# Performance work log

Hardware: AMD Instinct MI355X
Metric: run time of the kernel (lower is better)

The kernel has to match this reference:

```python
import jax, jax.numpy as jnp
import numpy as np
import math

B, S, E, H = 2, 1024, 2560, 32
D = E // H  # 80


def setup_inputs() -> dict:
    key = jax.random.key(0)
    ks = jax.random.split(key, 10)
    hidden_states = jax.random.normal(ks[0], (B, S, E), dtype=jnp.float32)
    Wqkv = jax.random.normal(ks[1], (E, 3 * E), dtype=jnp.float32) * 0.02
    bqkv = jnp.zeros((3 * E,), dtype=jnp.float32)
    Wproj = jax.random.normal(ks[2], (E, E), dtype=jnp.float32) * 0.02
    bproj = jnp.zeros((E,), dtype=jnp.float32)
    # gate matrices: hadamard, pauli_x, pauli_z (all real branches in torch code)
    hadamard = jnp.array([[1.0, 1.0], [1.0, -1.0]], dtype=jnp.float32) / math.sqrt(2.0)
    pauli_x = jnp.array([[0.0, 1.0], [1.0, 0.0]], dtype=jnp.float32)
    pauli_z = jnp.array([[1.0, 0.0], [0.0, -1.0]], dtype=jnp.float32)
    gate_mats = jnp.stack([hadamard, pauli_x, pauli_z])  # (3,2,2)
    # phase_rotation init is zeros in torch; randomize slightly for nontrivial numerics
    gate_phases = jax.random.normal(ks[3], (3, D), dtype=jnp.float32) * 0.1
    gate_amps = jnp.ones((3, D), dtype=jnp.float32)
    quantum_phase = jax.random.normal(ks[4], (H,), dtype=jnp.float32) * 0.1
    interference_strength = jnp.float32(0.8)
    return {
        'hidden_states': hidden_states, 'Wqkv': Wqkv, 'bqkv': bqkv,
        'Wproj': Wproj, 'bproj': bproj, 'gate_mats': gate_mats,
        'gate_phases': gate_phases, 'gate_amps': gate_amps,
        'quantum_phase': quantum_phase,
        'interference_strength': interference_strength,
    }


def _gate_coeffs(gate_mats, gate_phases, gate_amps):
    # QuantumGate fwd: stack([x*cos(p), x*sin(p)], -1) @ G, summed over last axis, * amp
    # => per-dim scalar coeff: (cos(p)*(g00+g01) + sin(p)*(g10+g11)) * amp
    row0 = gate_mats[:, 0, 0] + gate_mats[:, 0, 1]  # (3,)
    row1 = gate_mats[:, 1, 0] + gate_mats[:, 1, 1]  # (3,)
    return (jnp.cos(gate_phases) * row0[:, None] + jnp.sin(gate_phases) * row1[:, None]) * gate_amps  # (3, D)


def reference(hidden_states, Wqkv, bqkv, Wproj, bproj, gate_mats, gate_phases, gate_amps, quantum_phase, interference_strength):
    scale = D ** -0.5
    qkv = hidden_states @ Wqkv + bqkv  # (B,S,3E)
    q, k, v = jnp.split(qkv, 3, axis=-1)
    # (B,H,S,D)
    q = q.reshape(B, S, H, D).transpose(0, 2, 1, 3)
    k = k.reshape(B, S, H, D).transpose(0, 2, 1, 3)
    v = v.reshape(B, S, H, D).transpose(0, 2, 1, 3)

    attn_scores = jnp.einsum('bhqd,bhkd->bhqk', q, k) * scale

    coeffs = _gate_coeffs(gate_mats, gate_phases, gate_amps)  # (3,D)
    # quantum attention per gate: (q * coeff_i) @ k^T * scale
    qa = jnp.einsum('gd,bhqd,bhkd->gbhqk', coeffs, q, k) * scale  # (3,B,H,S,S)
    interference = (qa[0] * qa[1] + qa[0] * qa[2] + qa[1] * qa[2]) * interference_strength
    attn_scores = attn_scores + interference / 3.0

    attn_probs = jax.nn.softmax(attn_scores, axis=-1)
    attn_probs = attn_probs * jnp.cos(quantum_phase)[None, :, None, None]

    attn_output = jnp.einsum('bhqk,bhkd->bhqd', attn_probs, v)
    attn_output = attn_output.transpose(0, 2, 1, 3).reshape(B, S, E)
    return attn_output @ Wproj + bproj
```

## Files before the change

kernel.cpp:

```cpp
#include <hip/hip_runtime.h>
#include <hip/hip_bf16.h>
#include <math.h>

#define S_  1024
#define E_  2560
#define H_  32
#define D_  80
#define E3_ 7680
#define M_  2048
#define QK_ 5120

typedef short bf16x8 __attribute__((ext_vector_type(8)));
typedef float f32x4  __attribute__((ext_vector_type(4)));

static __device__ __forceinline__ float bf2f(unsigned short u) {
    unsigned int i = ((unsigned int)u) << 16;
    float f; __builtin_memcpy(&f, &i, 4); return f;
}
static __device__ __forceinline__ unsigned short f2bf(float f) {
    unsigned int i; __builtin_memcpy(&i, &f, 4);
    i += 0x7fffu + ((i >> 16) & 1u);
    return (unsigned short)(i >> 16);
}

static __device__ __forceinline__ void gload_lds16(
    const unsigned short* g, unsigned short* l)
{
    __builtin_amdgcn_global_load_lds(
        (const __attribute__((address_space(1))) void*)g,
        (__attribute__((address_space(3))) void*)l, 16, 0, 0);
}

__global__ __launch_bounds__(256) void cvt_bf16_kernel(
    const float* __restrict__ in, unsigned short* __restrict__ out, int n8)
{
    int i = (blockIdx.x * 256 + threadIdx.x);
    if (i >= n8) return;
    const float* p = in + (size_t)i * 8;
    float4 a = *(const float4*)p;
    float4 b = *(const float4*)(p + 4);
    union { uint4 v; unsigned short s[8]; } o;
    o.s[0]=f2bf(a.x); o.s[1]=f2bf(a.y); o.s[2]=f2bf(a.z); o.s[3]=f2bf(a.w);
    o.s[4]=f2bf(b.x); o.s[5]=f2bf(b.y); o.s[6]=f2bf(b.z); o.s[7]=f2bf(b.w);
    *(uint4*)(out + (size_t)i * 8) = o.v;
}

__global__ __launch_bounds__(256) void transpose_bf16_kernel(
    const float* __restrict__ in, unsigned short* __restrict__ out, int R, int C)
{
    __shared__ unsigned short tile[64][74];
    const int t  = threadIdx.x;
    const int r0 = blockIdx.y * 64, c0 = blockIdx.x * 64;
    const int rr = t >> 4;
    const int c4 = (t & 15) * 4;
#pragma unroll
    for (int p = 0; p < 4; ++p) {
        const int r = rr + p * 16;
        float4 v = *(const float4*)&in[(size_t)(r0 + r) * C + c0 + c4];
        tile[c4 + 0][r] = f2bf(v.x);
        tile[c4 + 1][r] = f2bf(v.y);
        tile[c4 + 2][r] = f2bf(v.z);
        tile[c4 + 3][r] = f2bf(v.w);
    }
    __syncthreads();
    const int orow = t >> 3;
    const int ocol = (t & 7) * 8;
#pragma unroll
    for (int p = 0; p < 2; ++p) {
        const int c = orow + p * 32;
        *(uint4*)&out[(size_t)(c0 + c) * R + r0 + ocol] = *(const uint4*)&tile[c][ocol];
    }
}

__global__ __launch_bounds__(512, 2) void mfma_gemm256_kernel(
    const unsigned short* __restrict__ A, int lda,
    const unsigned short* __restrict__ Wt,
    const float* __restrict__ bias,
    unsigned short* __restrict__ dst0, int sd0,
    unsigned short* __restrict__ dst1, int sd1, int ncut,
    int K)
{
    __shared__ unsigned short lds[2][2][256 * 64];

    const int t    = threadIdx.x;
    const int lane = t & 63, wave = t >> 6;
    const int quad = lane >> 4, l15 = lane & 15;
    const int wm   = wave >> 2, wn = wave & 3;
    const int m0   = blockIdx.y * 256;
    const int n0   = blockIdx.x * 256;

    const int pr = lane >> 3;
    const int ls = ((lane & 7) - pr) & 7;
    const unsigned short* gA[4];
    const unsigned short* gB[4];
#pragma unroll
    for (int i = 0; i < 4; ++i) {
        const int r = wave * 32 + i * 8 + pr;
        gA[i] = A  + (size_t)(m0 + r) * lda + ls * 8;
        gB[i] = Wt + (size_t)(n0 + r) * K   + ls * 8;
    }

    f32x4 acc[8][4];
#pragma unroll
    for (int mf = 0; mf < 8; ++mf)
#pragma unroll
        for (int nf = 0; nf < 4; ++nf) acc[mf][nf] = (f32x4){0.f, 0.f, 0.f, 0.f};

#pragma unroll
    for (int i = 0; i < 4; ++i) {
        gload_lds16(gA[i], &lds[0][0][(wave * 32 + i * 8) * 64]);
        gload_lds16(gB[i], &lds[0][1][(wave * 32 + i * 8) * 64]);
    }

    const int NT = K / 64;
    for (int kt = 0; kt < NT; ++kt) {
        __syncthreads();

        if (kt + 1 < NT) {
            const int nb = (kt + 1) & 1;
            const size_t koff = (size_t)(kt + 1) * 64;
#pragma unroll
            for (int i = 0; i < 4; ++i) {
                gload_lds16(gA[i] + koff, &lds[nb][0][(wave * 32 + i * 8) * 64]);
                gload_lds16(gB[i] + koff, &lds[nb][1][(wave * 32 + i * 8) * 64]);
            }
        }

        const unsigned short* As = &lds[kt & 1][0][0];
        const unsigned short* Bs = &lds[kt & 1][1][0];
#pragma unroll
        for (int kc = 0; kc < 2; ++kc) {
            bf16x8 bfr[4];
#pragma unroll
            for (int nf = 0; nf < 4; ++nf) {
                const int row = wn * 64 + nf * 16 + l15;
                const int ps  = (quad + 4 * kc + (row & 7)) & 7;
                bfr[nf] = *(const bf16x8*)&Bs[row * 64 + ps * 8];
            }
#pragma unroll
            for (int mf = 0; mf < 8; ++mf) {
                const int row = wm * 128 + mf * 16 + l15;
                const int ps  = (quad + 4 * kc + (row & 7)) & 7;
                const bf16x8 af = *(const bf16x8*)&As[row * 64 + ps * 8];
#pragma unroll
                for (int nf = 0; nf < 4; ++nf)
                    acc[mf][nf] = __builtin_amdgcn_mfma_f32_16x16x32_bf16(af, bfr[nf], acc[mf][nf], 0, 0, 0);
            }
        }
    }

#pragma unroll
    for (int nf = 0; nf < 4; ++nf) {
        const int col = n0 + wn * 64 + nf * 16 + l15;
        const float bv = bias[col];
        unsigned short* dst; int sd, cc;
        if (col < ncut) { dst = dst0; sd = sd0; cc = col; }
        else            { dst = dst1; sd = sd1; cc = col - ncut; }
#pragma unroll
        for (int mf = 0; mf < 8; ++mf) {
            const int rowb = m0 + wm * 128 + mf * 16 + quad * 4;
#pragma unroll
            for (int g = 0; g < 4; ++g)
                dst[(size_t)(rowb + g) * sd + cc] = f2bf(acc[mf][nf][g] + bv);
        }
    }
}

__global__ __launch_bounds__(512) void mfma_gemm_proj_kernel(
    const unsigned short* __restrict__ A, int lda,
    const unsigned short* __restrict__ Wt,
    const float* __restrict__ bias,
    float* __restrict__ dst, int sd,
    int K)
{
    __shared__ unsigned short lds[2][2][128 * 64];

    const int t    = threadIdx.x;
    const int lane = t & 63, wave = t >> 6;
    const int quad = lane >> 4, l15 = lane & 15;
    const int wm   = wave >> 2, wn = wave & 3;
    const int m0   = blockIdx.y * 128;
    const int n0   = blockIdx.x * 128;

    const int pr = lane >> 3;
    const int ls = ((lane & 7) - pr) & 7;
    const unsigned short* gA[2];
    const unsigned short* gB[2];
#pragma unroll
    for (int i = 0; i < 2; ++i) {
        const int r = wave * 16 + i * 8 + pr;
        gA[i] = A  + (size_t)(m0 + r) * lda + ls * 8;
        gB[i] = Wt + (size_t)(n0 + r) * K   + ls * 8;
    }

    f32x4 acc[4][2];
#pragma unroll
    for (int mf = 0; mf < 4; ++mf)
#pragma unroll
        for (int nf = 0; nf < 2; ++nf) acc[mf][nf] = (f32x4){0.f, 0.f, 0.f, 0.f};

#pragma unroll
    for (int i = 0; i < 2; ++i) {
        gload_lds16(gA[i], &lds[0][0][(wave * 16 + i * 8) * 64]);
        gload_lds16(gB[i], &lds[0][1][(wave * 16 + i * 8) * 64]);
    }

    const int NT = K / 64;
    for (int kt = 0; kt < NT; ++kt) {
        __syncthreads();

        if (kt + 1 < NT) {
            const int nb = (kt + 1) & 1;
            const size_t koff = (size_t)(kt + 1) * 64;
#pragma unroll
            for (int i = 0; i < 2; ++i) {
                gload_lds16(gA[i] + koff, &lds[nb][0][(wave * 16 + i * 8) * 64]);
                gload_lds16(gB[i] + koff, &lds[nb][1][(wave * 16 + i * 8) * 64]);
            }
        }

        const unsigned short* As = &lds[kt & 1][0][0];
        const unsigned short* Bs = &lds[kt & 1][1][0];
#pragma unroll
        for (int kc = 0; kc < 2; ++kc) {
            bf16x8 bfr[2];
#pragma unroll
            for (int nf = 0; nf < 2; ++nf) {
                const int row = wn * 32 + nf * 16 + l15;
                const int ps  = (quad + 4 * kc + (row & 7)) & 7;
                bfr[nf] = *(const bf16x8*)&Bs[row * 64 + ps * 8];
            }
#pragma unroll
            for (int mf = 0; mf < 4; ++mf) {
                const int row = wm * 64 + mf * 16 + l15;
                const int ps  = (quad + 4 * kc + (row & 7)) & 7;
                const bf16x8 af = *(const bf16x8*)&As[row * 64 + ps * 8];
#pragma unroll
                for (int nf = 0; nf < 2; ++nf)
                    acc[mf][nf] = __builtin_amdgcn_mfma_f32_16x16x32_bf16(af, bfr[nf], acc[mf][nf], 0, 0, 0);
            }
        }
    }

#pragma unroll
    for (int nf = 0; nf < 2; ++nf) {
        const int col = n0 + wn * 32 + nf * 16 + l15;
        const float bv = bias[col];
#pragma unroll
        for (int mf = 0; mf < 4; ++mf) {
            const int rowb = m0 + wm * 64 + mf * 16 + quad * 4;
#pragma unroll
            for (int g = 0; g < 4; ++g)
                dst[(size_t)(rowb + g) * sd + col] = acc[mf][nf][g] + bv;
        }
    }
}

__global__ __launch_bounds__(256, 2) void attn_mfma_kernel(
    unsigned short* __restrict__ qk,
    const unsigned short* __restrict__ vsrc,
    const float* __restrict__ gmats,
    const float* __restrict__ gphases,
    const float* __restrict__ gamps,
    const float* __restrict__ qphase,
    const float* __restrict__ is_ptr)
{
    __shared__ unsigned short Ks[64 * 104];
    __shared__ unsigned short Vt[80 * 72];
    __shared__ unsigned short Ps[64 * 72];
    __shared__ float cs[240];

    const int t    = threadIdx.x;
    const int wave = t >> 6, lane = t & 63;
    const int quad = lane >> 4, l15 = lane & 15;
    const int lin0 = blockIdx.x;
    const int lin  = ((lin0 & 7) << 7) | (lin0 >> 3);
    const int qt = lin & 15;
    const int bh = lin >> 4;
    const int h  = bh & 31;
    const int b  = bh >> 5;

    const float scale = 0.111803398874989485f;
    const float c2    = scale * scale * is_ptr[0] * (1.0f / 3.0f);
    const float cosph = cosf(qphase[h]);

    if (t < 240) {
        int g = t / 80;
        float r0 = gmats[g*4+0] + gmats[g*4+1];
        float r1 = gmats[g*4+2] + gmats[g*4+3];
        cs[t] = (cosf(gphases[t]) * r0 + sinf(gphases[t]) * r1) * gamps[t];
    }

    const int srow = t >> 2;
    const int scg  = (t & 3) * 20;

    const int vkg  = t & 15;
    const int vdg0 = t >> 4;

    {
        const unsigned short* qp = qk + (size_t)(b * S_ + qt * 64 + srow) * QK_ + h * D_ + scg;
#pragma unroll
        for (int u = 0; u < 5; ++u)
            *(ushort4*)&Ks[srow * 104 + scg + 4 * u] = *(const ushort4*)(qp + 4 * u);
        *(ushort4*)&Ks[srow * 104 + 80 + (t & 3) * 4] = (ushort4){0, 0, 0, 0};
    }
    __syncthreads();

    ushort4 kpre[5];
    ushort4 vpre[8];
    {
        const unsigned short* kp = qk + (size_t)(b * S_ + srow) * QK_ + E_ + h * D_ + scg;
#pragma unroll
        for (int u = 0; u < 5; ++u) kpre[u] = *(const ushort4*)(kp + 4 * u);
        const unsigned short* vb = vsrc + (size_t)(b * S_) * E_ + h * D_;
#pragma unroll
        for (int i = 0; i < 4; ++i)
            vpre[i] = *(const ushort4*)(vb + (size_t)(vkg * 4 + i) * E_ + vdg0 * 4);
        if (t < 64) {
#pragma unroll
            for (int i = 0; i < 4; ++i)
                vpre[4 + i] = *(const ushort4*)(vb + (size_t)(vkg * 4 + i) * E_ + 64 + vdg0 * 4);
        }
    }

    bf16x8 afq[3], afg[3][3];
#pragma unroll
    for (int kc = 0; kc < 3; ++kc)
        afq[kc] = *(const bf16x8*)&Ks[(wave * 16 + l15) * 104 + quad * 8 + kc * 32];
#pragma unroll
    for (int g = 0; g < 3; ++g)
#pragma unroll
        for (int kc = 0; kc < 3; ++kc)
#pragma unroll
            for (int j = 0; j < 8; ++j) {
                int d = kc * 32 + quad * 8 + j;
                float c = (d < 80) ? cs[g * 80 + d] : 0.f;
                afg[g][kc][j] = (short)f2bf(bf2f((unsigned short)afq[kc][j]) * c);
            }

    f32x4 Ov[5];
#pragma unroll
    for (int nf = 0; nf < 5; ++nf) Ov[nf] = (f32x4){0.f, 0.f, 0.f, 0.f};
    float m_r[4] = {-INFINITY, -INFINITY, -INFINITY, -INFINITY};
    float l_r[4] = {0.f, 0.f, 0.f, 0.f};

    for (int kt = 0; kt < 16; ++kt) {
        __syncthreads();

#pragma unroll
        for (int u = 0; u < 5; ++u)
            *(ushort4*)&Ks[srow * 104 + scg + 4 * u] = kpre[u];

        {
            const unsigned short rm[4][4] = {
                {vpre[0].x, vpre[0].y, vpre[0].z, vpre[0].w},
                {vpre[1].x, vpre[1].y, vpre[1].z, vpre[1].w},
                {vpre[2].x, vpre[2].y, vpre[2].z, vpre[2].w},
                {vpre[3].x, vpre[3].y, vpre[3].z, vpre[3].w}};
#pragma unroll
            for (int j = 0; j < 4; ++j) {
                ushort4 w = {rm[0][j], rm[1][j], rm[2][j], rm[3][j]};
                *(ushort4*)&Vt[(vdg0 * 4 + j) * 72 + vkg * 4] = w;
            }
        }
        if (t < 64) {
            const unsigned short rm[4][4] = {
                {vpre[4].x, vpre[4].y, vpre[4].z, vpre[4].w},
                {vpre[5].x, vpre[5].y, vpre[5].z, vpre[5].w},
                {vpre[6].x, vpre[6].y, vpre[6].z, vpre[6].w},
                {vpre[7].x, vpre[7].y, vpre[7].z, vpre[7].w}};
#pragma unroll
            for (int j = 0; j < 4; ++j) {
                ushort4 w = {rm[0][j], rm[1][j], rm[2][j], rm[3][j]};
                *(ushort4*)&Vt[(64 + vdg0 * 4 + j) * 72 + vkg * 4] = w;
            }
        }
        __syncthreads();

        if (kt < 15) {
            const unsigned short* kp = qk + (size_t)(b * S_ + (kt + 1) * 64 + srow) * QK_ + E_ + h * D_ + scg;
#pragma unroll
            for (int u = 0; u < 5; ++u) kpre[u] = *(const ushort4*)(kp + 4 * u);
            const unsigned short* vb = vsrc + (size_t)(b * S_ + (kt + 1) * 64) * E_ + h * D_;
#pragma unroll
            for (int i = 0; i < 4; ++i)
                vpre[i] = *(const ushort4*)(vb + (size_t)(vkg * 4 + i) * E_ + vdg0 * 4);
            if (t < 64) {
#pragma unroll
                for (int i = 0; i < 4; ++i)
                    vpre[4 + i] = *(const ushort4*)(vb + (size_t)(vkg * 4 + i) * E_ + 64 + vdg0 * 4);
            }
        }

        float p[4][4];
        float mx[4] = {-INFINITY, -INFINITY, -INFINITY, -INFINITY};
#pragma unroll
        for (int hf = 0; hf < 2; ++hf) {
            f32x4 sacc[4][2];
#pragma unroll
            for (int v = 0; v < 4; ++v)
#pragma unroll
                for (int n = 0; n < 2; ++n) sacc[v][n] = (f32x4){0.f, 0.f, 0.f, 0.f};
#pragma unroll
            for (int kc = 0; kc < 3; ++kc) {
                bf16x8 bk[2];
#pragma unroll
                for (int n = 0; n < 2; ++n)
                    bk[n] = *(const bf16x8*)&Ks[((hf * 2 + n) * 16 + l15) * 104 + quad * 8 + kc * 32];
#pragma unroll
                for (int n = 0; n < 2; ++n)
                    sacc[0][n] = __builtin_amdgcn_mfma_f32_16x16x32_bf16(afq[kc], bk[n], sacc[0][n], 0, 0, 0);
#pragma unroll
                for (int g = 0; g < 3; ++g)
#pragma unroll
                    for (int n = 0; n < 2; ++n)
                        sacc[1+g][n] = __builtin_amdgcn_mfma_f32_16x16x32_bf16(afg[g][kc], bk[n], sacc[1+g][n], 0, 0, 0);
            }
#pragma unroll
            for (int n = 0; n < 2; ++n)
#pragma unroll
                for (int r = 0; r < 4; ++r) {
                    float s0 = sacc[1][n][r], s1 = sacc[2][n][r], s2 = sacc[3][n][r];
                    float s = fmaf(fmaf(s0, s1, (s0 + s1) * s2), c2, sacc[0][n][r] * scale);
                    p[hf * 2 + n][r] = s;
                    mx[r] = fmaxf(mx[r], s);
                }
        }

#pragma unroll
        for (int r = 0; r < 4; ++r) {
            mx[r] = fmaxf(mx[r], __shfl_xor(mx[r], 1));
            mx[r] = fmaxf(mx[r], __shfl_xor(mx[r], 2));
            mx[r] = fmaxf(mx[r], __shfl_xor(mx[r], 4));
            mx[r] = fmaxf(mx[r], __shfl_xor(mx[r], 8));
        }
        float alpha[4];
#pragma unroll
        for (int r = 0; r < 4; ++r) {
            float m_new = fmaxf(m_r[r], mx[r]);
            alpha[r] = __expf(m_r[r] - m_new);
            m_r[r] = m_new;
        }
#pragma unroll
        for (int nf = 0; nf < 4; ++nf)
#pragma unroll
            for (int r = 0; r < 4; ++r)
                p[nf][r] = __expf(p[nf][r] - m_r[r]);
#pragma unroll
        for (int r = 0; r < 4; ++r) {
            float s = p[0][r] + p[1][r] + p[2][r] + p[3][r];
            s += __shfl_xor(s, 1);
            s += __shfl_xor(s, 2);
            s += __shfl_xor(s, 4);
            s += __shfl_xor(s, 8);
            l_r[r] = l_r[r] * alpha[r] + s;
        }

#pragma unroll
        for (int nf = 0; nf < 4; ++nf)
#pragma unroll
            for (int r = 0; r < 4; ++r)
                Ps[(wave * 16 + quad * 4 + r) * 72 + l15 + 16 * nf] = f2bf(p[nf][r]);
        __asm__ volatile("s_waitcnt lgkmcnt(0)" ::: "memory");

#pragma unroll
        for (int nf = 0; nf < 5; ++nf)
#pragma unroll
            for (int r = 0; r < 4; ++r) Ov[nf][r] *= alpha[r];

        bf16x8 ap[2];
#pragma unroll
        for (int kc = 0; kc < 2; ++kc)
            ap[kc] = *(const bf16x8*)&Ps[(wave * 16 + l15) * 72 + quad * 8 + kc * 32];
#pragma unroll
        for (int nf = 0; nf < 5; ++nf)
#pragma unroll
            for (int kc = 0; kc < 2; ++kc) {
                bf16x8 bv = *(const bf16x8*)&Vt[(nf * 16 + l15) * 72 + quad * 8 + kc * 32];
                Ov[nf] = __builtin_amdgcn_mfma_f32_16x16x32_bf16(ap[kc], bv, Ov[nf], 0, 0, 0);
            }
    }

    float inv[4];
#pragma unroll
    for (int r = 0; r < 4; ++r) inv[r] = cosph / l_r[r];
#pragma unroll
    for (int nf = 0; nf < 5; ++nf)
#pragma unroll
        for (int r = 0; r < 4; ++r)
            qk[(size_t)(b * S_ + qt * 64 + wave * 16 + quad * 4 + r) * QK_ + h * D_ + nf * 16 + l15]
                = f2bf(Ov[nf][r] * inv[r]);
}

extern "C" void kernel_launch(void* const* d_in, const int* in_sizes, int n_in,
                              void* d_out, int out_size, void* d_ws, size_t ws_size,
                              hipStream_t stream) {
    (void)in_sizes; (void)n_in; (void)out_size; (void)ws_size;
    const float* hidden  = (const float*)d_in[0];
    const float* Wqkv    = (const float*)d_in[1];
    const float* bqkv    = (const float*)d_in[2];
    const float* Wproj   = (const float*)d_in[3];
    const float* bproj   = (const float*)d_in[4];
    const float* gmats   = (const float*)d_in[5];
    const float* gphases = (const float*)d_in[6];
    const float* gamps   = (const float*)d_in[7];
    const float* qphase  = (const float*)d_in[8];
    const float* is_ptr  = (const float*)d_in[9];

    unsigned short* qk_ws  = (unsigned short*)d_ws;
    unsigned short* h_bf16 = (unsigned short*)((char*)d_ws + (size_t)M_ * QK_ * 2);
    unsigned short* Wt     = (unsigned short*)((char*)d_ws + (size_t)M_ * QK_ * 2 + (size_t)M_ * E_ * 2);
    unsigned short* v_buf  = (unsigned short*)d_out;

    dim3 blk(256);
    cvt_bf16_kernel<<<dim3((M_ * E_ / 8 + 255) / 256), blk, 0, stream>>>(hidden, h_bf16, M_ * E_ / 8);
    transpose_bf16_kernel<<<dim3(E3_/64, E_/64), blk, 0, stream>>>(Wqkv, Wt, E_, E3_);
    mfma_gemm256_kernel<<<dim3(E3_/256, M_/256), dim3(512), 0, stream>>>(
        h_bf16, E_, Wt, bqkv, qk_ws, QK_, v_buf, E_, QK_, E_);
    attn_mfma_kernel<<<dim3(2 * H_ * (S_/64)), blk, 0, stream>>>(
        qk_ws, v_buf, gmats, gphases, gamps, qphase, is_ptr);
    transpose_bf16_kernel<<<dim3(E_/64, E_/64), blk, 0, stream>>>(Wproj, Wt, E_, E_);
    mfma_gemm_proj_kernel<<<dim3(E_/128, M_/128), dim3(512), 0, stream>>>(
        qk_ws, QK_, Wt, bproj, (float*)d_out, E_, E_);
}
```

Baseline: 388.4 us.

## Prefetch two K-tiles ahead with partial vmcnt waits in both GEMMs

Both bf16 MFMA GEMM kernels now keep two K tiles in flight instead of one. Before the loop they issue loads for tiles 0 and 1. Each iteration computes, barriers, issues the load for tile kt+2 into the buffer just freed, then uses s_waitcnt vmcnt(N) so it waits only for the older load before the next barrier. The aim is to stop draining all outstanding global-to-LDS loads at every __syncthreads and so hide more memory latency. It depends on hand-counted vmcnt values and explicit barriers, which is fragile if the compiler emits other vector memory operations.

```diff
diff --git a/kernel.cpp b/kernel.cpp
--- a/kernel.cpp
+++ b/kernel.cpp
@@ -106,26 +106,26 @@
 #pragma unroll
         for (int nf = 0; nf < 4; ++nf) acc[mf][nf] = (f32x4){0.f, 0.f, 0.f, 0.f};
 
+    const int NT = K / 64;
+
 #pragma unroll
     for (int i = 0; i < 4; ++i) {
         gload_lds16(gA[i], &lds[0][0][(wave * 32 + i * 8) * 64]);
         gload_lds16(gB[i], &lds[0][1][(wave * 32 + i * 8) * 64]);
     }
-
-    const int NT = K / 64;
+    if (NT > 1) {
+#pragma unroll
+        for (int i = 0; i < 4; ++i) {
+            gload_lds16(gA[i] + 64, &lds[1][0][(wave * 32 + i * 8) * 64]);
+            gload_lds16(gB[i] + 64, &lds[1][1][(wave * 32 + i * 8) * 64]);
+        }
+        __asm__ volatile("s_waitcnt vmcnt(8)" ::: "memory");
+    } else {
+        __asm__ volatile("s_waitcnt vmcnt(0)" ::: "memory");
+    }
+    __builtin_amdgcn_s_barrier();
+
     for (int kt = 0; kt < NT; ++kt) {
-        __syncthreads();
-
-        if (kt + 1 < NT) {
-            const int nb = (kt + 1) & 1;
-            const size_t koff = (size_t)(kt + 1) * 64;
-#pragma unroll
-            for (int i = 0; i < 4; ++i) {
-                gload_lds16(gA[i] + koff, &lds[nb][0][(wave * 32 + i * 8) * 64]);
-                gload_lds16(gB[i] + koff, &lds[nb][1][(wave * 32 + i * 8) * 64]);
-            }
-        }
-
         const unsigned short* As = &lds[kt & 1][0][0];
         const unsigned short* Bs = &lds[kt & 1][1][0];
 #pragma unroll
@@ -146,6 +146,24 @@
                 for (int nf = 0; nf < 4; ++nf)
                     acc[mf][nf] = __builtin_amdgcn_mfma_f32_16x16x32_bf16(af, bfr[nf], acc[mf][nf], 0, 0, 0);
             }
+        }
+
+        __builtin_amdgcn_s_barrier();
+
+        if (kt + 2 < NT) {
+            const size_t koff = (size_t)(kt + 2) * 64;
+#pragma unroll
+            for (int i = 0; i < 4; ++i) {
+                gload_lds16(gA[i] + koff, &lds[kt & 1][0][(wave * 32 + i * 8) * 64]);
+                gload_lds16(gB[i] + koff, &lds[kt & 1][1][(wave * 32 + i * 8) * 64]);
+            }
+        }
+        if (kt + 1 < NT) {
+            if (kt + 2 < NT)
+                __asm__ volatile("s_waitcnt vmcnt(8)" ::: "memory");
+            else
+                __asm__ volatile("s_waitcnt vmcnt(0)" ::: "memory");
+            __builtin_amdgcn_s_barrier();
         }
     }
 
@@ -199,26 +217,26 @@
 #pragma unroll
         for (int nf = 0; nf < 2; ++nf) acc[mf][nf] = (f32x4){0.f, 0.f, 0.f, 0.f};
 
+    const int NT = K / 64;
+
 #pragma unroll
     for (int i = 0; i < 2; ++i) {
         gload_lds16(gA[i], &lds[0][0][(wave * 16 + i * 8) * 64]);
         gload_lds16(gB[i], &lds[0][1][(wave * 16 + i * 8) * 64]);
     }
-
-    const int NT = K / 64;
+    if (NT > 1) {
+#pragma unroll
+        for (int i = 0; i < 2; ++i) {
+            gload_lds16(gA[i] + 64, &lds[1][0][(wave * 16 + i * 8) * 64]);
+            gload_lds16(gB[i] + 64, &lds[1][1][(wave * 16 + i * 8) * 64]);
+        }
+        __asm__ volatile("s_waitcnt vmcnt(4)" ::: "memory");
+    } else {
+        __asm__ volatile("s_waitcnt vmcnt(0)" ::: "memory");
+    }
+    __builtin_amdgcn_s_barrier();
+
     for (int kt = 0; kt < NT; ++kt) {
-        __syncthreads();
-
-        if (kt + 1 < NT) {
-            const int nb = (kt + 1) & 1;
-            const size_t koff = (size_t)(kt + 1) * 64;
-#pragma unroll
-            for (int i = 0; i < 2; ++i) {
-                gload_lds16(gA[i] + koff, &lds[nb][0][(wave * 16 + i * 8) * 64]);
-                gload_lds16(gB[i] + koff, &lds[nb][1][(wave * 16 + i * 8) * 64]);
-            }
-        }
-
         const unsigned short* As = &lds[kt & 1][0][0];
         const unsigned short* Bs = &lds[kt & 1][1][0];
 #pragma unroll
@@ -239,6 +257,24 @@
                 for (int nf = 0; nf < 2; ++nf)
                     acc[mf][nf] = __builtin_amdgcn_mfma_f32_16x16x32_bf16(af, bfr[nf], acc[mf][nf], 0, 0, 0);
             }
+        }
+
+        __builtin_amdgcn_s_barrier();
+
+        if (kt + 2 < NT) {
+            const size_t koff = (size_t)(kt + 2) * 64;
+#pragma unroll
+            for (int i = 0; i < 2; ++i) {
+                gload_lds16(gA[i] + koff, &lds[kt & 1][0][(wave * 16 + i * 8) * 64]);
+                gload_lds16(gB[i] + koff, &lds[kt & 1][1][(wave * 16 + i * 8) * 64]);
+            }
+        }
+        if (kt + 1 < NT) {
+            if (kt + 2 < NT)
+                __asm__ volatile("s_waitcnt vmcnt(4)" ::: "memory");
+            else
+                __asm__ volatile("s_waitcnt vmcnt(0)" ::: "memory");
+            __builtin_amdgcn_s_barrier();
         }
     }
 
```

Measured after the change: 407.3 us. 4.9% more time.
